# Optimization experiments

Measured on AMD Instinct MI355X. Metric: run time of the kernel, lower is better.

Reference implementation:

```python
import jax, jax.numpy as jnp
import numpy as np

SOS = 4998
EOS = 4999
SCALING = 2.0


def setup_inputs() -> dict:
    key = jax.random.key(0)
    ks = jax.random.split(key, 12)
    B, T, E, D, A, C, F, ODIM, L = 32, 1000, 512, 1024, 512, 10, 100, 5000, 100
    s = 0.02
    return {
        "hpad": jax.random.normal(ks[0], (B, T, E), jnp.float32),
        "ys": jax.random.randint(ks[1], (B, L), 0, SOS, jnp.int32),
        # AttLoc params
        "w_enc": jax.random.normal(ks[2], (A, E), jnp.float32) * s,
        "b_enc": jnp.zeros((A,), jnp.float32),
        "w_dec": jax.random.normal(ks[3], (A, D), jnp.float32) * s,
        "w_att": jax.random.normal(ks[4], (A, C), jnp.float32) * s,
        "w_conv": jax.random.normal(ks[5], (C, 1, 2 * F + 1), jnp.float32) * s,  # OIH 1D conv kernel
        "w_gvec": jax.random.normal(ks[6], (1, A), jnp.float32) * s,
        "b_gvec": jnp.zeros((1,), jnp.float32),
        # Decoder params
        "embed": jax.random.normal(ks[7], (ODIM, D), jnp.float32) * s,
        "w_ih": jax.random.normal(ks[8], (4 * D, D + E), jnp.float32) * s,
        "w_hh": jax.random.normal(ks[9], (4 * D, D), jnp.float32) * s,
        "b_ih": jnp.zeros((4 * D,), jnp.float32),
        "b_hh": jnp.zeros((4 * D,), jnp.float32),
        "w_out": jax.random.normal(ks[10], (ODIM, D), jnp.float32) * s,
        "b_out": jnp.zeros((ODIM,), jnp.float32),
    }


def _decode(hpad, ys, w_enc, b_enc, w_dec, w_att, w_conv, w_gvec, b_gvec,
            embed, w_ih, w_hh, b_ih, b_hh, w_out, b_out):
    B, T, E = hpad.shape
    D = w_hh.shape[1]
    F = (w_conv.shape[-1] - 1) // 2
    # ys_in = [sos; y] per utterance (all same length -> already padded)
    ys_in = jnp.concatenate([jnp.full((B, 1), SOS, ys.dtype), ys], axis=1)  # [B, olen]
    eys = embed[ys_in]                                                      # [B, olen, D]
    # pre_compute_enc_h = mlp_enc(enc_h)
    pre = jnp.einsum('bte,ae->bta', hpad, w_enc) + b_enc                    # [B, T, A]
    att0 = jnp.full((B, T), 1.0 / T, hpad.dtype)   # uniform init attention (all hlen == T)
    z0 = jnp.zeros((B, D), hpad.dtype)
    c0 = jnp.zeros((B, D), hpad.dtype)

    def step(carry, ey_i):
        z, c, aw = carry
        # location-aware conv over previous attention weights: [B,1,T] -> [B,C,T]
        conv = jax.lax.conv_general_dilated(aw[:, None, :], w_conv, (1,), [(F, F)],
                                            dimension_numbers=('NCH', 'OIH', 'NCH'))
        att_feat = jnp.einsum('bct,ac->bta', conv, w_att)                   # mlp_att
        dec = (z @ w_dec.T)[:, None, :]                                     # mlp_dec, tiled
        e = jnp.tanh(att_feat + pre + dec) @ w_gvec[0] + b_gvec[0]          # [B, T]
        w = jax.nn.softmax(SCALING * e, axis=1)
        ctx = jnp.einsum('bt,bte->be', w, hpad)                             # [B, E]
        # LSTMCell
        x = jnp.concatenate([ey_i, ctx], axis=1)                            # [B, D+E]
        gates = x @ w_ih.T + b_ih + z @ w_hh.T + b_hh
        i_g, f_g, g_g, o_g = jnp.split(gates, 4, axis=1)
        c_new = jax.nn.sigmoid(f_g) * c + jax.nn.sigmoid(i_g) * jnp.tanh(g_g)
        z_new = jax.nn.sigmoid(o_g) * jnp.tanh(c_new)
        return (z_new, c_new, w), z_new

    _, z_all = jax.lax.scan(step, (z0, c0, att0), jnp.swapaxes(eys, 0, 1))  # [olen, B, D]
    y_all = jnp.einsum('obd,vd->obv', z_all, w_out) + b_out                 # [olen, B, odim]
    return jnp.swapaxes(y_all, 0, 1)                                        # [B, olen, odim]


def reference(hpad, ys, w_enc, b_enc, w_dec, w_att, w_conv, w_gvec, b_gvec,
              embed, w_ih, w_hh, b_ih, b_hh, w_out, b_out):
    return _decode(hpad, ys, w_enc, b_enc, w_dec, w_att, w_conv, w_gvec, b_gvec,
                   embed, w_ih, w_hh, b_ih, b_hh, w_out, b_out)
```

## Files before the change

### kernel.cpp

```cpp
#include <hip/hip_runtime.h>
#include <math.h>

#define B_    32
#define T_    1000
#define E_    512
#define D_    1024
#define A_    512
#define C_    10
#define F_    100
#define ODIM_ 5000
#define OLEN_ 101
#define SOS_  4998

#define OFF_PRE   0u
#define N_PREF    (32u*512u*1000u/2u)
#define OFF_HPB   (OFF_PRE + N_PREF)
#define N_HPBF    (32u*1000u*512u/2u)
#define OFF_DEC   (OFF_HPB + N_HPBF)
#define N_DEC     (32u*512u)
#define OFF_CONV  (OFF_DEC + N_DEC)
#define N_CONVB   (32u*10u*1000u)
#define OFF_AW    (OFF_CONV + N_CONVB)
#define N_AW      (32u*1000u)
#define OFF_S     (OFF_AW + N_AW)
#define N_S       (64u)
#define OFF_CTX   (OFF_S + N_S)
#define N_CTX     (32u*512u)
#define OFF_GP    (OFF_CTX + N_CTX)
#define N_GP      (8u*32u*4096u)
#define OFF_Z     (OFF_GP + N_GP)
#define N_Z       (32u*1024u)
#define OFF_C     (OFF_Z + N_Z)
#define OFF_ZALL  (OFF_C + N_Z)

__device__ __forceinline__ float fast_tanh(float x) {
    float cx = fminf(8.f, fmaxf(-8.f, x));
    float e = __expf(2.f * cx);
    return (e - 1.f) * __builtin_amdgcn_rcpf(e + 1.f);
}
__device__ __forceinline__ float fast_sigmoid(float x) {
    float cx = fminf(30.f, fmaxf(-30.f, x));
    return __builtin_amdgcn_rcpf(1.f + __expf(-cx));
}

__device__ __forceinline__ unsigned bf16rne(float f) {
    unsigned u = __float_as_uint(f);
    return (u + 0x7fffu + ((u >> 16) & 1u)) >> 16;
}
__device__ __forceinline__ unsigned packbf(float lo, float hi) {
    return bf16rne(lo) | (bf16rne(hi) << 16);
}
__device__ __forceinline__ float bflo(unsigned u) { return __uint_as_float(u << 16); }
__device__ __forceinline__ float bfhi(unsigned u) { return __uint_as_float(u & 0xffff0000u); }

__global__ __launch_bounds__(256) void k_init(float* ws) {
    int i = blockIdx.x * 256 + threadIdx.x;
    if (i < (int)N_Z) { ws[OFF_Z + i] = 0.f; ws[OFF_C + i] = 0.f; }
    if (i < (int)N_CTX) ws[OFF_CTX + i] = 0.f;
    if (i < (int)N_AW) ws[OFF_AW + i] = 1.0f;
    if (i < 64) ws[OFF_S + i] = (i >= 32) ? 1000.f : 0.f;
}

__global__ __launch_bounds__(256) void k_hp16(const float* __restrict__ hp, float* ws) {
    uint2* hpb = (uint2*)(ws + OFF_HPB);
    const float4* src = (const float4*)hp;
    for (unsigned i = blockIdx.x * 256 + threadIdx.x; i < 4096000u; i += 4000u * 256u) {
        float4 v = src[i];
        uint2 o;
        o.x = packbf(v.x, v.y);
        o.y = packbf(v.z, v.w);
        hpb[i] = o;
    }
}

__global__ __launch_bounds__(256) void k_pre_t(const float* __restrict__ hp,
                                               const float* __restrict__ we,
                                               const float* __restrict__ be,
                                               float* ws) {
    __shared__ float As[64][68];
    __shared__ float Bs[64][68];
    unsigned short* preb = (unsigned short*)(ws + OFF_PRE);
    int bt = blockIdx.y;
    int b = bt >> 4, tc = bt & 15;
    int t0 = tc * 64;
    int n0 = blockIdx.x * 64;
    int tid = threadIdx.x;
    int tr = tid >> 4, tcl = tid & 15;
    float acc[4][4] = {};
    for (int k0 = 0; k0 < 512; k0 += 64) {
        for (int i = tid; i < 1024; i += 256) {
            int m = i >> 4, kq = (i & 15) << 2;
            int t = t0 + m;
            float4 v = (t < 1000) ? *(const float4*)&hp[((size_t)(b * 1000 + t)) * 512 + k0 + kq]
                                  : make_float4(0.f, 0.f, 0.f, 0.f);
            As[kq + 0][m] = v.x; As[kq + 1][m] = v.y; As[kq + 2][m] = v.z; As[kq + 3][m] = v.w;
            float4 w = *(const float4*)&we[(size_t)(n0 + m) * 512 + k0 + kq];
            Bs[kq + 0][m] = w.x; Bs[kq + 1][m] = w.y; Bs[kq + 2][m] = w.z; Bs[kq + 3][m] = w.w;
        }
        __syncthreads();
        #pragma unroll 16
        for (int kk = 0; kk < 64; ++kk) {
            float4 av = *(const float4*)&As[kk][tr << 2];
            float4 bv = *(const float4*)&Bs[kk][tcl << 2];
            float a[4] = {av.x, av.y, av.z, av.w};
            float bq[4] = {bv.x, bv.y, bv.z, bv.w};
            #pragma unroll
            for (int i = 0; i < 4; i++)
                #pragma unroll
                for (int j = 0; j < 4; j++) acc[i][j] += a[i] * bq[j];
        }
        __syncthreads();
    }
    int tt = t0 + (tr << 2);
    if (tt < 1000) {
        #pragma unroll
        for (int j = 0; j < 4; ++j) {
            int a = n0 + (tcl << 2) + j;
            float bea = be[a];
            uint2 o;
            o.x = packbf(acc[0][j] + bea, acc[1][j] + bea);
            o.y = packbf(acc[2][j] + bea, acc[3][j] + bea);
            *(uint2*)&preb[((size_t)(b * 512 + a)) * 1000 + tt] = o;
        }
    }
}

__global__ __launch_bounds__(256, 2) void k_prep(const float* __restrict__ wdec,
                                                 const float* __restrict__ wconv,
                                                 const float* __restrict__ wih,
                                                 const float* __restrict__ whh,
                                                 const float* __restrict__ embed,
                                                 const int* __restrict__ ys,
                                                 float* ws, int step) {
    int tid = threadIdx.x;
    if (blockIdx.x < 1024) {
        int u = blockIdx.x;
        if (u < 64) ws[OFF_CTX + u * 256 + tid] = 0.f;
        if (u == 64 && tid < 32) ws[OFF_S + (step & 1) * 32 + tid] = 0.f;
        int w = u * 4 + (tid >> 6);
        int lane = tid & 63;
        int a = w >> 3, bg7 = w & 7;
        const float4* wr = (const float4*)(wdec + (size_t)a * 1024);
        float4 w4[4];
        #pragma unroll
        for (int i = 0; i < 4; i++) w4[i] = wr[i * 64 + lane];
        float acc[4] = {0.f, 0.f, 0.f, 0.f};
        #pragma unroll
        for (int bb = 0; bb < 4; ++bb) {
            const float4* zr = (const float4*)(ws + OFF_Z + (size_t)(bg7 * 4 + bb) * 1024);
            #pragma unroll
            for (int i = 0; i < 4; i++) {
                float4 z4 = zr[i * 64 + lane];
                acc[bb] += w4[i].x * z4.x + w4[i].y * z4.y + w4[i].z * z4.z + w4[i].w * z4.w;
            }
        }
        #pragma unroll
        for (int off = 32; off > 0; off >>= 1) {
            acc[0] += __shfl_xor(acc[0], off, 64);
            acc[1] += __shfl_xor(acc[1], off, 64);
            acc[2] += __shfl_xor(acc[2], off, 64);
            acc[3] += __shfl_xor(acc[3], off, 64);
        }
        if (lane == 0) {
            #pragma unroll
            for (int bb = 0; bb < 4; ++bb)
                ws[OFF_DEC + (bg7 * 4 + bb) * 512 + a] = acc[bb];
        }
    } else if (blockIdx.x < 1344) {
        int blk = blockIdx.x - 1024;
        int b = blk / 10, c = blk - b * 10;
        if (tid >= 250) return;
        float invS = __builtin_amdgcn_rcpf(ws[OFF_S + ((step + 1) & 1) * 32 + b]);
        int t = tid * 4;
        const float* ar = ws + OFF_AW + b * 1000;
        const float* wc = wconv + c * 201;
        float a0, a1, a2, a3;
        a0 = (t - 100 >= 0) ? ar[t - 100] : 0.f;
        a1 = (t -  99 >= 0) ? ar[t -  99] : 0.f;
        a2 = (t -  98 >= 0) ? ar[t -  98] : 0.f;
        a3 = (t -  97 >= 0) ? ar[t -  97] : 0.f;
        float c0 = 0.f, c1 = 0.f, c2 = 0.f, c3 = 0.f;
        #pragma unroll 4
        for (int j = 0; j < 201; ++j) {
            float w = wc[j];
            c0 += a0 * w; c1 += a1 * w; c2 += a2 * w; c3 += a3 * w;
            a0 = a1; a1 = a2; a2 = a3;
            int ni = t + j - 96;
            a3 = (ni >= 0 && ni < 1000) ? ar[ni] : 0.f;
        }
        float* o = ws + OFF_CONV + (size_t)(b * 10 + c) * 1000 + t;
        o[0] = c0 * invS; o[1] = c1 * invS; o[2] = c2 * invS; o[3] = c3 * invS;
    } else {
        __shared__ float wlds[32][132];
        __shared__ float xs[32][36];
        int blk = blockIdx.x - 1344;
        int nt = blk & 31, ks = blk >> 5;
        int n0 = nt * 128;
        bool isE = (ks < 4);
        int kloc = isE ? ks * 256 : (ks - 4) * 256;
        int r = tid >> 1, h = tid & 1;
        int bx = tid >> 3, q8 = tid & 7;
        int tok = (step == 0) ? SOS_ : ys[bx * 100 + step - 1];
        const float* xsrc = isE ? (embed + (size_t)tok * 1024 + kloc)
                                : (ws + OFF_Z + (size_t)bx * 1024 + kloc);
        int nq = tid & 31, bq = tid >> 5;
        float acc[4][4] = {};
        for (int kc = 0; kc < 8; ++kc) {
            int koff = kc * 32;
            {
                const float* wrow = isE ? (wih + (size_t)(n0 + r) * 1536 + kloc + koff + h * 16)
                                        : (whh + (size_t)(n0 + r) * 1024 + kloc + koff + h * 16);
                #pragma unroll
                for (int j = 0; j < 4; ++j) {
                    float4 v = *(const float4*)&wrow[j * 4];
                    int kb = h * 16 + j * 4;
                    wlds[kb + 0][r] = v.x; wlds[kb + 1][r] = v.y;
                    wlds[kb + 2][r] = v.z; wlds[kb + 3][r] = v.w;
                }
            }
            {
                float4 v = *(const float4*)&xsrc[koff + q8 * 4];
                xs[q8 * 4 + 0][bx] = v.x; xs[q8 * 4 + 1][bx] = v.y;
                xs[q8 * 4 + 2][bx] = v.z; xs[q8 * 4 + 3][bx] = v.w;
            }
            __syncthreads();
            #pragma unroll 8
            for (int kk = 0; kk < 32; ++kk) {
                float4 wv = *(const float4*)&wlds[kk][nq * 4];
                float4 xv = *(const float4*)&xs[kk][bq * 4];
                float wa[4] = {wv.x, wv.y, wv.z, wv.w};
                float xa[4] = {xv.x, xv.y, xv.z, xv.w};
                #pragma unroll
                for (int i = 0; i < 4; i++)
                    #pragma unroll
                    for (int j = 0; j < 4; j++) acc[i][j] += wa[i] * xa[j];
            }
            __syncthreads();
        }
        float* gp = ws + OFF_GP + (size_t)(ks * 32 + bq * 4) * 4096 + n0 + nq * 4;
        #pragma unroll
        for (int j = 0; j < 4; j++)
            #pragma unroll
            for (int i = 0; i < 4; i++)
                gp[(size_t)j * 4096 + i] = acc[i][j];
    }
}

__global__ __launch_bounds__(512, 2) void k_ectx(const float* __restrict__ watt,
                                                 const float* __restrict__ gvec,
                                                 const float* __restrict__ bgv,
                                                 float* ws, int step) {
    __shared__ float sa[512 * 12];
    __shared__ float part[1024];
    __shared__ float wsh[128];
    const unsigned short* preb = (const unsigned short*)(ws + OFF_PRE);
    const unsigned short* hpb  = (const unsigned short*)(ws + OFF_HPB);
    int b = blockIdx.x >> 3, tc = blockIdx.x & 7;
    int tbase = tc * 128;
    int tid = threadIdx.x;
    {
        const float* wrow = watt + tid * 10;
        float* d = sa + tid * 12;
        #pragma unroll
        for (int c = 0; c < 10; ++c) d[c] = wrow[c];
        d[10] = gvec[tid];
        d[11] = ws[OFF_DEC + b * 512 + tid];
    }
    __syncthreads();
    int w = tid >> 6, l = tid & 63;
    int t = tbase + l * 2;
    bool valid = (t < 1000);
    float2 cvv[10];
    const float* convb = ws + OFF_CONV + b * 10000;
    #pragma unroll
    for (int c = 0; c < 10; ++c)
        cvv[c] = valid ? *(const float2*)&convb[c * 1000 + t] : make_float2(0.f, 0.f);
    int a0 = w * 64;
    const unsigned short* pt = preb + ((size_t)(b * 512 + a0)) * 1000 + t;
    float ex = 0.f, ey = 0.f;
    #pragma unroll 8
    for (int a = a0; a < a0 + 64; ++a) {
        unsigned u = valid ? *(const unsigned*)pt : 0u;
        pt += 1000;
        const float4* sp = (const float4*)(sa + a * 12);
        float4 w0 = sp[0];
        float4 w1 = sp[1];
        float4 w2 = sp[2];
        float px = bflo(u), py = bfhi(u);
        float sx = px + w2.w, sy = py + w2.w;
        sx += cvv[0].x * w0.x; sy += cvv[0].y * w0.x;
        sx += cvv[1].x * w0.y; sy += cvv[1].y * w0.y;
        sx += cvv[2].x * w0.z; sy += cvv[2].y * w0.z;
        sx += cvv[3].x * w0.w; sy += cvv[3].y * w0.w;
        sx += cvv[4].x * w1.x; sy += cvv[4].y * w1.x;
        sx += cvv[5].x * w1.y; sy += cvv[5].y * w1.y;
        sx += cvv[6].x * w1.z; sy += cvv[6].y * w1.z;
        sx += cvv[7].x * w1.w; sy += cvv[7].y * w1.w;
        sx += cvv[8].x * w2.x; sy += cvv[8].y * w2.x;
        sx += cvv[9].x * w2.y; sy += cvv[9].y * w2.y;
        ex += w2.z * fast_tanh(sx);
        ey += w2.z * fast_tanh(sy);
    }
    part[w * 128 + l * 2]     = ex;
    part[w * 128 + l * 2 + 1] = ey;
    __syncthreads();
    float wtil = 0.f;
    if (tid < 128) {
        int tt = tbase + tid;
        float e = 0.f;
        #pragma unroll
        for (int j = 0; j < 8; ++j) e += part[j * 128 + tid];
        if (tt < 1000) {
            wtil = __expf(2.f * (e + bgv[0]));
            ws[OFF_AW + b * 1000 + tt] = wtil;
        }
        wsh[tid] = wtil;
    }
    __syncthreads();
    part[tid] = wtil;
    __syncthreads();
    for (int off = 256; off >= 1; off >>= 1) {
        if (tid < off) part[tid] += part[tid + off];
        __syncthreads();
    }
    if (tid == 0) atomicAdd(&ws[OFF_S + (step & 1) * 32 + b], part[0]);
    int e4 = tid & 127, th = tid >> 7;
    int lt0 = th * 32;
    int ltend = lt0 + 32;
    int tmax = 1000 - tbase; if (ltend > tmax) ltend = tmax;
    float4 acc = make_float4(0.f, 0.f, 0.f, 0.f);
    for (int lt = lt0; lt < ltend; ++lt) {
        float wv = wsh[lt];
        uint2 hu = *(const uint2*)&hpb[((size_t)(b * 1000 + tbase + lt)) * 512 + e4 * 4];
        acc.x += wv * bflo(hu.x); acc.y += wv * bfhi(hu.x);
        acc.z += wv * bflo(hu.y); acc.w += wv * bfhi(hu.y);
    }
    float* cx = ws + OFF_CTX + b * 512 + e4 * 4;
    atomicAdd(cx + 0, acc.x); atomicAdd(cx + 1, acc.y);
    atomicAdd(cx + 2, acc.z); atomicAdd(cx + 3, acc.w);
}

__global__ __launch_bounds__(256, 2) void k_gl(const float* __restrict__ wih,
                                               const float* __restrict__ bih,
                                               const float* __restrict__ bhh,
                                               float* ws, int step) {
    __shared__ float wlds[32][20];
    __shared__ float xs[32][33];
    __shared__ float glb[16][33];
    __shared__ float sinv[32];
    int tid = threadIdx.x;
    int d0 = blockIdx.x * 4;
    if (tid < 32) sinv[tid] = __builtin_amdgcn_rcpf(ws[OFF_S + (step & 1) * 32 + tid]);
    __syncthreads();
    int r = tid >> 4, h = tid & 15;
    int ng_r = (r >> 2) * 1024 + d0 + (r & 3);
    const float* wrow = wih + (size_t)ng_r * 1536 + 1024 + h * 2;
    int bx = tid >> 3, q8 = tid & 7;
    const float* xsrc = ws + OFF_CTX + (size_t)bx * 512 + q8 * 4;
    float xscale = sinv[bx];
    int nq = tid & 7, bq = tid >> 3;
    float acc[2] = {0.f, 0.f};
    for (int kc = 0; kc < 16; ++kc) {
        int k0 = kc * 32;
        {
            float2 v = *(const float2*)&wrow[k0];
            wlds[h * 2 + 0][r] = v.x;
            wlds[h * 2 + 1][r] = v.y;
        }
        {
            float4 v = *(const float4*)&xsrc[k0];
            xs[q8 * 4 + 0][bx] = v.x * xscale; xs[q8 * 4 + 1][bx] = v.y * xscale;
            xs[q8 * 4 + 2][bx] = v.z * xscale; xs[q8 * 4 + 3][bx] = v.w * xscale;
        }
        __syncthreads();
        #pragma unroll 8
        for (int kk = 0; kk < 32; ++kk) {
            float w0 = wlds[kk][nq * 2], w1 = wlds[kk][nq * 2 + 1];
            float x  = xs[kk][bq];
            acc[0] += w0 * x;
            acc[1] += w1 * x;
        }
        __syncthreads();
    }
    #pragma unroll
    for (int i = 0; i < 2; ++i) {
        int nl = nq * 2 + i;
        int ng = (nl >> 2) * 1024 + d0 + (nl & 3);
        float s = acc[i] + bih[ng] + bhh[ng];
        #pragma unroll
        for (int sl = 0; sl < 8; ++sl)
            s += ws[OFF_GP + (size_t)(sl * 32 + bq) * 4096 + ng];
        glb[nl][bq] = s;
    }
    __syncthreads();
    if (tid < 128) {
        int dl = tid >> 5, b = tid & 31;
        float gi = glb[dl][b];
        float gf = glb[4 + dl][b];
        float gg = glb[8 + dl][b];
        float go = glb[12 + dl][b];
        int id = b * 1024 + d0 + dl;
        float c_old = ws[OFF_C + id];
        float si = fast_sigmoid(gi);
        float sf = fast_sigmoid(gf);
        float so = fast_sigmoid(go);
        float cn = sf * c_old + si * fast_tanh(gg);
        float hh = so * fast_tanh(cn);
        ws[OFF_C + id] = cn;
        ws[OFF_Z + id] = hh;
        ws[OFF_ZALL + ((size_t)step * 32 + b) * 1024 + d0 + dl] = hh;
    }
}

__global__ __launch_bounds__(256) void k_out(const float* __restrict__ zall,
                                             const float* __restrict__ wo,
                                             const float* __restrict__ bo,
                                             float* __restrict__ out) {
    __shared__ float As[64][68];
    __shared__ float Bs[64][68];
    int m0 = blockIdx.y * 64, n0 = blockIdx.x * 64;
    int tid = threadIdx.x;
    int tr = tid >> 4, tc = tid & 15;
    float acc[4][4] = {};
    for (int k0 = 0; k0 < 1024; k0 += 64) {
        for (int i = tid; i < 1024; i += 256) {
            int m = i >> 4, kq = (i & 15) << 2;
            int gm = m0 + m;
            float4 v = (gm < 3232) ? *(const float4*)&zall[(size_t)gm * 1024 + k0 + kq]
                                   : make_float4(0.f, 0.f, 0.f, 0.f);
            As[kq + 0][m] = v.x; As[kq + 1][m] = v.y; As[kq + 2][m] = v.z; As[kq + 3][m] = v.w;
            int gn = n0 + m;
            float4 w = (gn < 5000) ? *(const float4*)&wo[(size_t)gn * 1024 + k0 + kq]
                                   : make_float4(0.f, 0.f, 0.f, 0.f);
            Bs[kq + 0][m] = w.x; Bs[kq + 1][m] = w.y; Bs[kq + 2][m] = w.z; Bs[kq + 3][m] = w.w;
        }
        __syncthreads();
        #pragma unroll 16
        for (int kk = 0; kk < 64; ++kk) {
            float4 av = *(const float4*)&As[kk][tr << 2];
            float4 bv = *(const float4*)&Bs[kk][tc << 2];
            float a[4] = {av.x, av.y, av.z, av.w};
            float b[4] = {bv.x, bv.y, bv.z, bv.w};
            #pragma unroll
            for (int i = 0; i < 4; i++)
                #pragma unroll
                for (int j = 0; j < 4; j++) acc[i][j] += a[i] * b[j];
        }
        __syncthreads();
    }
    #pragma unroll
    for (int i = 0; i < 4; i++) {
        int m = m0 + (tr << 2) + i;
        if (m >= 3232) continue;
        int b = m & 31, o = m >> 5;
        #pragma unroll
        for (int j = 0; j < 4; j++) {
            int v = n0 + (tc << 2) + j;
            if (v < 5000)
                out[((size_t)b * 101 + o) * 5000 + v] = acc[i][j] + bo[v];
        }
    }
}

extern "C" void kernel_launch(void* const* d_in, const int* in_sizes, int n_in,
                              void* d_out, int out_size, void* d_ws, size_t ws_size,
                              hipStream_t stream) {
    const float* hpad   = (const float*)d_in[0];
    const int*   ys     = (const int*)d_in[1];
    const float* w_enc  = (const float*)d_in[2];
    const float* b_enc  = (const float*)d_in[3];
    const float* w_dec  = (const float*)d_in[4];
    const float* w_att  = (const float*)d_in[5];
    const float* w_conv = (const float*)d_in[6];
    const float* w_gvec = (const float*)d_in[7];
    const float* b_gvec = (const float*)d_in[8];
    const float* embed  = (const float*)d_in[9];
    const float* w_ih   = (const float*)d_in[10];
    const float* w_hh   = (const float*)d_in[11];
    const float* b_ih   = (const float*)d_in[12];
    const float* b_hh   = (const float*)d_in[13];
    const float* w_out  = (const float*)d_in[14];
    const float* b_out  = (const float*)d_in[15];
    float* ws  = (float*)d_ws;
    float* out = (float*)d_out;

    k_init<<<128, 256, 0, stream>>>(ws);
    k_hp16<<<4000, 256, 0, stream>>>(hpad, ws);
    k_pre_t<<<dim3(8, 512), 256, 0, stream>>>(hpad, w_enc, b_enc, ws);

    for (int step = 0; step < OLEN_; ++step) {
        k_prep<<<1600, 256, 0, stream>>>(w_dec, w_conv, w_ih, w_hh, embed, ys, ws, step);
        k_ectx<<<256, 512, 0, stream>>>(w_att, w_gvec, b_gvec, ws, step);
        k_gl<<<256, 256, 0, stream>>>(w_ih, b_ih, b_hh, ws, step);
    }

    k_out<<<dim3(79, 51), 256, 0, stream>>>(ws + OFF_ZALL, w_out, b_out, out);
}
```

Before: 10.19 ms.

## Pre-pack attention params per batch, shuffle-reduce sums, enlarge output GEMM tiles

Attention weights, gvec and the per-step decoder projection are now packed once into a per-batch 12-float record in global memory. The energy kernel reads them with wave-uniform loads instead of staging them into shared memory each step, which drops one barrier and the LDS fill. The block-wide sum for the softmax denominator now uses wave shuffles instead of a nine-stage shared-memory tree. The final output projection GEMM moves from 64x64 tiles with 4x4 per-thread work to 128x128 tiles with 8x8 per-thread work, raising arithmetic intensity at the cost of more registers and fewer blocks.

```diff
diff --git a/kernel.cpp b/kernel.cpp
--- a/kernel.cpp
+++ b/kernel.cpp
@@ -16,9 +16,9 @@
 #define N_PREF    (32u*512u*1000u/2u)
 #define OFF_HPB   (OFF_PRE + N_PREF)
 #define N_HPBF    (32u*1000u*512u/2u)
-#define OFF_DEC   (OFF_HPB + N_HPBF)
-#define N_DEC     (32u*512u)
-#define OFF_CONV  (OFF_DEC + N_DEC)
+#define OFF_PP    (OFF_HPB + N_HPBF)
+#define N_PP      (32u*512u*12u)
+#define OFF_CONV  (OFF_PP + N_PP)
 #define N_CONVB   (32u*10u*1000u)
 #define OFF_AW    (OFF_CONV + N_CONVB)
 #define N_AW      (32u*1000u)
@@ -29,9 +29,9 @@
 #define OFF_GP    (OFF_CTX + N_CTX)
 #define N_GP      (8u*32u*4096u)
 #define OFF_Z     (OFF_GP + N_GP)
-#define N_Z       (32u*1024u)
-#define OFF_C     (OFF_Z + N_Z)
-#define OFF_ZALL  (OFF_C + N_Z)
+#define N_Z1      (32u*1024u)
+#define OFF_C     (OFF_Z + N_Z1)
+#define OFF_ZALL  (OFF_C + N_Z1)
 
 __device__ __forceinline__ float fast_tanh(float x) {
     float cx = fminf(8.f, fmaxf(-8.f, x));
@@ -53,12 +53,21 @@
 __device__ __forceinline__ float bflo(unsigned u) { return __uint_as_float(u << 16); }
 __device__ __forceinline__ float bfhi(unsigned u) { return __uint_as_float(u & 0xffff0000u); }
 
-__global__ __launch_bounds__(256) void k_init(float* ws) {
+__global__ __launch_bounds__(256) void k_init(const float* __restrict__ watt,
+                                              const float* __restrict__ gvec,
+                                              float* ws) {
     int i = blockIdx.x * 256 + threadIdx.x;
-    if (i < (int)N_Z) { ws[OFF_Z + i] = 0.f; ws[OFF_C + i] = 0.f; }
+    if (i < (int)N_Z1) { ws[OFF_Z + i] = 0.f; ws[OFF_C + i] = 0.f; }
     if (i < (int)N_CTX) ws[OFF_CTX + i] = 0.f;
     if (i < (int)N_AW) ws[OFF_AW + i] = 1.0f;
     if (i < 64) ws[OFF_S + i] = (i >= 32) ? 1000.f : 0.f;
+    if (i < 16384) {
+        int a = i & 511;
+        float* d = ws + OFF_PP + (size_t)i * 12;
+        #pragma unroll
+        for (int c = 0; c < 10; ++c) d[c] = watt[a * 10 + c];
+        d[10] = gvec[a];
+    }
 }
 
 __global__ __launch_bounds__(256) void k_hp16(const float* __restrict__ hp, float* ws) {
@@ -164,7 +173,7 @@
         if (lane == 0) {
             #pragma unroll
             for (int bb = 0; bb < 4; ++bb)
-                ws[OFF_DEC + (bg7 * 4 + bb) * 512 + a] = acc[bb];
+                ws[OFF_PP + ((size_t)((bg7 * 4 + bb) * 512 + a)) * 12 + 11] = acc[bb];
         }
     } else if (blockIdx.x < 1344) {
         int blk = blockIdx.x - 1024;
@@ -246,11 +255,8 @@
     }
 }
 
-__global__ __launch_bounds__(512, 2) void k_ectx(const float* __restrict__ watt,
-                                                 const float* __restrict__ gvec,
-                                                 const float* __restrict__ bgv,
+__global__ __launch_bounds__(512, 2) void k_ectx(const float* __restrict__ bgv,
                                                  float* ws, int step) {
-    __shared__ float sa[512 * 12];
     __shared__ float part[1024];
     __shared__ float wsh[128];
     const unsigned short* preb = (const unsigned short*)(ws + OFF_PRE);
@@ -258,16 +264,8 @@
     int b = blockIdx.x >> 3, tc = blockIdx.x & 7;
     int tbase = tc * 128;
     int tid = threadIdx.x;
-    {
-        const float* wrow = watt + tid * 10;
-        float* d = sa + tid * 12;
-        #pragma unroll
-        for (int c = 0; c < 10; ++c) d[c] = wrow[c];
-        d[10] = gvec[tid];
-        d[11] = ws[OFF_DEC + b * 512 + tid];
-    }
-    __syncthreads();
     int w = tid >> 6, l = tid & 63;
+    int wu = __builtin_amdgcn_readfirstlane(w);
     int t = tbase + l * 2;
     bool valid = (t < 1000);
     float2 cvv[10];
@@ -275,31 +273,30 @@
     #pragma unroll
     for (int c = 0; c < 10; ++c)
         cvv[c] = valid ? *(const float2*)&convb[c * 1000 + t] : make_float2(0.f, 0.f);
-    int a0 = w * 64;
-    const unsigned short* pt = preb + ((size_t)(b * 512 + a0)) * 1000 + t;
+    const float* pb = ws + OFF_PP + ((size_t)(b * 512 + wu * 64)) * 12;
+    const unsigned short* pt = preb + ((size_t)(b * 512 + wu * 64)) * 1000 + t;
     float ex = 0.f, ey = 0.f;
     #pragma unroll 8
-    for (int a = a0; a < a0 + 64; ++a) {
+    for (int i = 0; i < 64; ++i) {
         unsigned u = valid ? *(const unsigned*)pt : 0u;
         pt += 1000;
-        const float4* sp = (const float4*)(sa + a * 12);
-        float4 w0 = sp[0];
-        float4 w1 = sp[1];
-        float4 w2 = sp[2];
+        float4 q0 = *(const float4*)(pb + i * 12);
+        float4 q1 = *(const float4*)(pb + i * 12 + 4);
+        float4 q2 = *(const float4*)(pb + i * 12 + 8);
         float px = bflo(u), py = bfhi(u);
-        float sx = px + w2.w, sy = py + w2.w;
-        sx += cvv[0].x * w0.x; sy += cvv[0].y * w0.x;
-        sx += cvv[1].x * w0.y; sy += cvv[1].y * w0.y;
-        sx += cvv[2].x * w0.z; sy += cvv[2].y * w0.z;
-        sx += cvv[3].x * w0.w; sy += cvv[3].y * w0.w;
-        sx += cvv[4].x * w1.x; sy += cvv[4].y * w1.x;
-        sx += cvv[5].x * w1.y; sy += cvv[5].y * w1.y;
-        sx += cvv[6].x * w1.z; sy += cvv[6].y * w1.z;
-        sx += cvv[7].x * w1.w; sy += cvv[7].y * w1.w;
-        sx += cvv[8].x * w2.x; sy += cvv[8].y * w2.x;
-        sx += cvv[9].x * w2.y; sy += cvv[9].y * w2.y;
-        ex += w2.z * fast_tanh(sx);
-        ey += w2.z * fast_tanh(sy);
+        float sx = px + q2.w, sy = py + q2.w;
+        sx += cvv[0].x * q0.x; sy += cvv[0].y * q0.x;
+        sx += cvv[1].x * q0.y; sy += cvv[1].y * q0.y;
+        sx += cvv[2].x * q0.z; sy += cvv[2].y * q0.z;
+        sx += cvv[3].x * q0.w; sy += cvv[3].y * q0.w;
+        sx += cvv[4].x * q1.x; sy += cvv[4].y * q1.x;
+        sx += cvv[5].x * q1.y; sy += cvv[5].y * q1.y;
+        sx += cvv[6].x * q1.z; sy += cvv[6].y * q1.z;
+        sx += cvv[7].x * q1.w; sy += cvv[7].y * q1.w;
+        sx += cvv[8].x * q2.x; sy += cvv[8].y * q2.x;
+        sx += cvv[9].x * q2.y; sy += cvv[9].y * q2.y;
+        ex += q2.z * fast_tanh(sx);
+        ey += q2.z * fast_tanh(sy);
     }
     part[w * 128 + l * 2]     = ex;
     part[w * 128 + l * 2 + 1] = ey;
@@ -317,13 +314,14 @@
         wsh[tid] = wtil;
     }
     __syncthreads();
-    part[tid] = wtil;
+    if (tid < 128) {
+        float ss = wtil;
+        #pragma unroll
+        for (int off = 32; off > 0; off >>= 1) ss += __shfl_xor(ss, off, 64);
+        if ((tid & 63) == 0) part[tid >> 6] = ss;
+    }
     __syncthreads();
-    for (int off = 256; off >= 1; off >>= 1) {
-        if (tid < off) part[tid] += part[tid + off];
-        __syncthreads();
-    }
-    if (tid == 0) atomicAdd(&ws[OFF_S + (step & 1) * 32 + b], part[0]);
+    if (tid == 0) atomicAdd(&ws[OFF_S + (step & 1) * 32 + b], part[0] + part[1]);
     int e4 = tid & 127, th = tid >> 7;
     int lt0 = th * 32;
     int ltend = lt0 + 32;
@@ -416,46 +414,56 @@
                                              const float* __restrict__ wo,
                                              const float* __restrict__ bo,
                                              float* __restrict__ out) {
-    __shared__ float As[64][68];
-    __shared__ float Bs[64][68];
-    int m0 = blockIdx.y * 64, n0 = blockIdx.x * 64;
+    __shared__ float As[16][132];
+    __shared__ float Bs[16][132];
+    int m0 = blockIdx.y * 128, n0 = blockIdx.x * 128;
     int tid = threadIdx.x;
-    int tr = tid >> 4, tc = tid & 15;
-    float acc[4][4] = {};
-    for (int k0 = 0; k0 < 1024; k0 += 64) {
-        for (int i = tid; i < 1024; i += 256) {
-            int m = i >> 4, kq = (i & 15) << 2;
-            int gm = m0 + m;
-            float4 v = (gm < 3232) ? *(const float4*)&zall[(size_t)gm * 1024 + k0 + kq]
-                                   : make_float4(0.f, 0.f, 0.f, 0.f);
-            As[kq + 0][m] = v.x; As[kq + 1][m] = v.y; As[kq + 2][m] = v.z; As[kq + 3][m] = v.w;
-            int gn = n0 + m;
-            float4 w = (gn < 5000) ? *(const float4*)&wo[(size_t)gn * 1024 + k0 + kq]
-                                   : make_float4(0.f, 0.f, 0.f, 0.f);
-            Bs[kq + 0][m] = w.x; Bs[kq + 1][m] = w.y; Bs[kq + 2][m] = w.z; Bs[kq + 3][m] = w.w;
+    int tx = tid & 15, ty = tid >> 4;
+    float acc[8][8] = {};
+    int ar = tid >> 1, ah = (tid & 1) * 8;
+    for (int k0 = 0; k0 < 1024; k0 += 16) {
+        {
+            int gm = m0 + ar;
+            float4 a0, a1;
+            if (gm < 3232) {
+                a0 = *(const float4*)&zall[(size_t)gm * 1024 + k0 + ah];
+                a1 = *(const float4*)&zall[(size_t)gm * 1024 + k0 + ah + 4];
+            } else { a0 = a1 = make_float4(0.f, 0.f, 0.f, 0.f); }
+            As[ah + 0][ar] = a0.x; As[ah + 1][ar] = a0.y; As[ah + 2][ar] = a0.z; As[ah + 3][ar] = a0.w;
+            As[ah + 4][ar] = a1.x; As[ah + 5][ar] = a1.y; As[ah + 6][ar] = a1.z; As[ah + 7][ar] = a1.w;
+            int gn = n0 + ar;
+            float4 b0, b1;
+            if (gn < 5000) {
+                b0 = *(const float4*)&wo[(size_t)gn * 1024 + k0 + ah];
+                b1 = *(const float4*)&wo[(size_t)gn * 1024 + k0 + ah + 4];
+            } else { b0 = b1 = make_float4(0.f, 0.f, 0.f, 0.f); }
+            Bs[ah + 0][ar] = b0.x; Bs[ah + 1][ar] = b0.y; Bs[ah + 2][ar] = b0.z; Bs[ah + 3][ar] = b0.w;
+            Bs[ah + 4][ar] = b1.x; Bs[ah + 5][ar] = b1.y; Bs[ah + 6][ar] = b1.z; Bs[ah + 7][ar] = b1.w;
         }
         __syncthreads();
-        #pragma unroll 16
-        for (int kk = 0; kk < 64; ++kk) {
-            float4 av = *(const float4*)&As[kk][tr << 2];
-            float4 bv = *(const float4*)&Bs[kk][tc << 2];
-            float a[4] = {av.x, av.y, av.z, av.w};
-            float b[4] = {bv.x, bv.y, bv.z, bv.w};
+        #pragma unroll
+        for (int kk = 0; kk < 16; ++kk) {
+            float4 a0v = *(const float4*)&As[kk][ty * 8];
+            float4 a1v = *(const float4*)&As[kk][ty * 8 + 4];
+            float4 b0v = *(const float4*)&Bs[kk][tx * 8];
+            float4 b1v = *(const float4*)&Bs[kk][tx * 8 + 4];
+            float am[8] = {a0v.x, a0v.y, a0v.z, a0v.w, a1v.x, a1v.y, a1v.z, a1v.w};
+            float bn[8] = {b0v.x, b0v.y, b0v.z, b0v.w, b1v.x, b1v.y, b1v.z, b1v.w};
             #pragma unroll
-            for (int i = 0; i < 4; i++)
+            for (int i = 0; i < 8; i++)
                 #pragma unroll
-                for (int j = 0; j < 4; j++) acc[i][j] += a[i] * b[j];
+                for (int j = 0; j < 8; j++) acc[i][j] += am[i] * bn[j];
         }
         __syncthreads();
     }
     #pragma unroll
-    for (int i = 0; i < 4; i++) {
-        int m = m0 + (tr << 2) + i;
+    for (int i = 0; i < 8; i++) {
+        int m = m0 + ty * 8 + i;
         if (m >= 3232) continue;
         int b = m & 31, o = m >> 5;
         #pragma unroll
-        for (int j = 0; j < 4; j++) {
-            int v = n0 + (tc << 2) + j;
+        for (int j = 0; j < 8; j++) {
+            int v = n0 + tx * 8 + j;
             if (v < 5000)
                 out[((size_t)b * 101 + o) * 5000 + v] = acc[i][j] + bo[v];
         }
@@ -484,15 +492,15 @@
     float* ws  = (float*)d_ws;
     float* out = (float*)d_out;
 
-    k_init<<<128, 256, 0, stream>>>(ws);
+    k_init<<<128, 256, 0, stream>>>(w_att, w_gvec, ws);
     k_hp16<<<4000, 256, 0, stream>>>(hpad, ws);
     k_pre_t<<<dim3(8, 512), 256, 0, stream>>>(hpad, w_enc, b_enc, ws);
 
     for (int step = 0; step < OLEN_; ++step) {
         k_prep<<<1600, 256, 0, stream>>>(w_dec, w_conv, w_ih, w_hh, embed, ys, ws, step);
-        k_ectx<<<256, 512, 0, stream>>>(w_att, w_gvec, b_gvec, ws, step);
+        k_ectx<<<256, 512, 0, stream>>>(b_gvec, ws, step);
         k_gl<<<256, 256, 0, stream>>>(w_ih, b_ih, b_hh, ws, step);
     }
 
-    k_out<<<dim3(79, 51), 256, 0, stream>>>(ws + OFF_ZALL, w_out, b_out, out);
-}
+    k_out<<<dim3(40, 26), 256, 0, stream>>>(ws + OFF_ZALL, w_out, b_out, out);
+}
```

Result: faster. 9.958 ms (-2.3%).
